# Optimization experiments

Measured on AMD Instinct MI355X. Metric: run time of the kernel, lower is better.

Reference implementation:

```python
import jax, jax.numpy as jnp
import numpy as np

N, E, D_IN, D, L = 50000, 100000, 78, 768, 5
BN_EPS = 1e-5


def setup_inputs() -> dict:
    key = jax.random.key(0)
    ks = jax.random.split(key, 8)
    s_in = 1.0 / np.sqrt(D_IN)
    s_d = 1.0 / np.sqrt(D)
    return {
        "x": jax.random.normal(ks[0], (N, D_IN), dtype=jnp.float32),
        "edge_index": jax.random.randint(ks[1], (2, E), 0, N, dtype=jnp.int32),
        "in_w": jax.random.normal(ks[2], (D_IN, D), dtype=jnp.float32) * s_in,
        "in_b": jnp.zeros((D,), jnp.float32),
        "conv_w": jax.random.normal(ks[3], (L, D, D), dtype=jnp.float32) * s_d,
        "conv_b": jnp.zeros((L, D), jnp.float32),
        "bn_g": jnp.ones((L, D), jnp.float32),
        "bn_b": jnp.zeros((L, D), jnp.float32),
        "out_w": jax.random.normal(ks[4], (D, D), dtype=jnp.float32) * s_d,
        "out_b": jnp.zeros((D,), jnp.float32),
    }


def reference(x, edge_index, in_w, in_b, conv_w, conv_b, bn_g, bn_b, out_w, out_b):
    src, dst = edge_index[0], edge_index[1]
    # GCN symmetric normalization with self-loops: deg over dst (col), +1 for self-loop
    deg = jax.ops.segment_sum(jnp.ones((E,), x.dtype), dst, num_segments=N) + 1.0
    dinv = jax.lax.rsqrt(deg)                      # deg >= 1, always finite
    edge_norm = (dinv[src] * dinv[dst])[:, None]   # [E, 1]
    self_norm = (dinv * dinv)[:, None]             # [N, 1] self-loop coefficient

    h = x @ in_w + in_b                            # input_proj -> [N, D]
    for l in range(L):
        xw = h @ conv_w[l]                         # GCNConv linear
        agg = jax.ops.segment_sum(xw[src] * edge_norm, dst, num_segments=N)
        agg = agg + xw * self_norm + conv_b[l]     # self-loop message + bias
        # BatchNorm1d (training mode: batch stats, biased variance)
        mu = jnp.mean(agg, axis=0)
        var = jnp.mean(jnp.square(agg - mu), axis=0)
        hn = (agg - mu) * jax.lax.rsqrt(var + BN_EPS) * bn_g[l] + bn_b[l]
        h = h + jax.nn.relu(hn)                    # residual (drop_ratio=0)
    return h @ out_w + out_b
```

## Files before the change

### kernel.cpp

```cpp
#include <hip/hip_runtime.h>
#include <hip/hip_bf16.h>
#include <stdint.h>

#define NN 50000
#define EE 100000
#define DD 768
#define MP 50176
#define KIN 96
#define SCB 196

typedef _Float16 half_t;
typedef __attribute__((ext_vector_type(8))) _Float16 v8h;
typedef __attribute__((ext_vector_type(4))) float v4f;

__device__ __forceinline__ void gload16(const half_t* g, half_t* l){
  __builtin_amdgcn_global_load_lds(
      (const __attribute__((address_space(1))) unsigned int*)(g),
      (__attribute__((address_space(3))) unsigned int*)(l),
      16, 0, 0);
}

template<int MODE, int KK>
__global__ __launch_bounds__(256, 3)
void gemm_t(const half_t* __restrict__ A,
            const half_t* __restrict__ Bt,
            const float* __restrict__ bias,
            float* __restrict__ o32,
            half_t* __restrict__ o16)
{
  constexpr int NKT = KK/32;
  __shared__ __align__(16) half_t lds[3*8192];

  const int nwg = gridDim.x;
  const int q = nwg >> 3, r = nwg & 7;
  const int xcd = blockIdx.x & 7, ii = blockIdx.x >> 3;
  const int L = (xcd < r ? xcd*(q+1) : r*(q+1) + (xcd-r)*q) + ii;
  const int rowb = L / 6, colb = L - rowb*6;
  const int m0 = rowb*128, n0 = colb*128;

  const int t = threadIdx.x, l = t&63, w = t>>6;
  const int wm = w>>1, wn = w&1;

  v4f acc[4][4];
  #pragma unroll
  for (int i=0;i<4;++i)
    #pragma unroll
    for (int j=0;j<4;++j){ v4f z = {0.f,0.f,0.f,0.f}; acc[i][j]=z; }

  const int srow = 16*w + (l>>2);
  const int sch  = ((l&3) ^ ((l>>3)&3))*8;
  const half_t* ApA = A  + (size_t)(m0 + srow)*KK + sch;
  const half_t* ApB = Bt + (size_t)(n0 + srow)*KK + sch;
  const int aoff = w*512;

  auto STAGE = [&](int kt2, int b){
    half_t* Ab = lds + b*8192;
    half_t* Bb = Ab + 4096;
    const int ko = kt2*32;
    gload16(ApA + ko,                  Ab + aoff);
    gload16(ApA + ko + (size_t)64*KK,  Ab + aoff + 2048);
    gload16(ApB + ko,                  Bb + aoff);
    gload16(ApB + ko + (size_t)64*KK,  Bb + aoff + 2048);
  };

  const int ra = l&15;
  const int pc = ((l>>4) ^ ((ra>>1)&3))*8;

  v8h af[2][4], bf[2][4];

  #define LOADF(s_, base_) do{                                              \
    const half_t* Ab_ = lds + (base_);                                      \
    const half_t* Bb_ = Ab_ + 4096;                                         \
    _Pragma("unroll")                                                       \
    for (int n_=0;n_<4;++n_) bf[s_][n_] = *(const v8h*)(Bb_ + (wn*64 + n_*16 + ra)*32 + pc); \
    _Pragma("unroll")                                                       \
    for (int m_=0;m_<4;++m_) af[s_][m_] = *(const v8h*)(Ab_ + (wm*64 + m_*16 + ra)*32 + pc); \
  }while(0)

  #define MFMAS(s_) do{                                                     \
    __builtin_amdgcn_s_setprio(1);                                          \
    _Pragma("unroll")                                                       \
    for (int m_=0;m_<4;++m_)                                                \
      _Pragma("unroll")                                                     \
      for (int n_=0;n_<4;++n_)                                              \
        acc[m_][n_] = __builtin_amdgcn_mfma_f32_16x16x32_f16(af[s_][m_], bf[s_][n_], acc[m_][n_], 0,0,0); \
    __builtin_amdgcn_s_setprio(0);                                          \
  }while(0)

  STAGE(0,0); STAGE(1,1); STAGE(2,2);
  asm volatile("s_waitcnt vmcnt(8)" ::: "memory");
  __builtin_amdgcn_s_barrier();
  LOADF(0, 0);
  asm volatile("s_waitcnt lgkmcnt(0)" ::: "memory");
  __builtin_amdgcn_sched_barrier(0);

  #pragma unroll
  for (int i=0;i<NKT;++i){
    const int cur = i&1, nxt = cur^1;
    if (i < NKT-1){
      if (i < NKT-2) asm volatile("s_waitcnt vmcnt(4)" ::: "memory");
      else           asm volatile("s_waitcnt vmcnt(0)" ::: "memory");
      __builtin_amdgcn_s_barrier();
      if (i+3 < NKT) STAGE(i+3, i%3);
      LOADF(nxt, ((i+1)%3)*8192);
      MFMAS(cur);
      asm volatile("s_waitcnt lgkmcnt(0)" ::: "memory");
      __builtin_amdgcn_sched_barrier(0);
    } else {
      MFMAS(cur);
    }
  }
  #undef LOADF
  #undef MFMAS

  if (MODE==2){
    float bv[4];
    #pragma unroll
    for (int n=0;n<4;++n) bv[n] = bias[n0 + wn*64 + n*16 + ra];
    #pragma unroll
    for (int m=0;m<4;++m){
      #pragma unroll
      for (int rr=0;rr<4;++rr){
        int row = m0 + wm*64 + m*16 + (l>>4)*4 + rr;
        if (row >= NN) continue;
        #pragma unroll
        for (int n=0;n<4;++n){
          int col = n0 + wn*64 + n*16 + ra;
          o32[(size_t)row*DD + col] = acc[m][n][rr] + bv[n];
        }
      }
    }
  } else {
    __syncthreads();
    #pragma unroll
    for (int m=0;m<4;++m){
      #pragma unroll
      for (int rr=0;rr<4;++rr){
        int row = wm*64 + m*16 + (l>>4)*4 + rr;
        #pragma unroll
        for (int n=0;n<4;++n){
          int col = wn*64 + n*16 + ra;
          float v = acc[m][n][rr];
          if (MODE==0) v += bias[n0+col];
          int gran = (col>>3) ^ (row&7);
          lds[row*128 + gran*8 + (col&7)] = (half_t)v;
        }
      }
    }
    __syncthreads();
    #pragma unroll
    for (int g=0; g<8; ++g){
      int row = (t>>4) + g*16;
      int gran = t&15;
      v8h hv = *(const v8h*)(lds + row*128 + ((gran ^ (row&7)))*8);
      *(v8h*)(o16 + (size_t)(m0+row)*DD + n0 + gran*8) = hv;
    }
  }
}

__global__ void k_count(const int* __restrict__ dst, int* __restrict__ cnt){
  int e = blockIdx.x*256 + threadIdx.x;
  if (e < EE) atomicAdd(&cnt[dst[e]], 1);
}
__global__ void k_dinv(const int* __restrict__ cnt, float* __restrict__ dinv){
  int i = blockIdx.x*256 + threadIdx.x;
  if (i < MP) dinv[i] = (i < NN) ? rsqrtf((float)cnt[i] + 1.0f) : 0.f;
}
__global__ void k_bsum(const int* __restrict__ cnt, int* __restrict__ bsum){
  int i = blockIdx.x*256 + threadIdx.x;
  int v = (i < NN) ? cnt[i] : 0;
  #pragma unroll
  for (int o=1;o<64;o<<=1) v += __shfl_xor(v, o);
  __shared__ int ws_[4];
  if ((threadIdx.x&63)==0) ws_[threadIdx.x>>6] = v;
  __syncthreads();
  if (threadIdx.x==0) bsum[blockIdx.x] = ws_[0]+ws_[1]+ws_[2]+ws_[3];
}
__global__ void k_btop(const int* __restrict__ bsum, int* __restrict__ boff){
  if (threadIdx.x==0){
    int run = 0;
    for (int b=0;b<SCB;++b){ boff[b] = run; run += bsum[b]; }
  }
}
__global__ void k_rowptr(const int* __restrict__ cnt, const int* __restrict__ boff,
                         int* __restrict__ rowptr, int* __restrict__ cursor){
  __shared__ int sh[256];
  int i = blockIdx.x*256 + threadIdx.x;
  int v = (i < NN) ? cnt[i] : 0;
  sh[threadIdx.x] = v; __syncthreads();
  #pragma unroll
  for (int o=1;o<256;o<<=1){
    int add = 0;
    if (threadIdx.x >= o) add = sh[threadIdx.x - o];
    __syncthreads();
    sh[threadIdx.x] += add;
    __syncthreads();
  }
  int excl = sh[threadIdx.x] - v + boff[blockIdx.x];
  if (i <= NN) rowptr[i] = excl;
  if (i < NN)  cursor[i] = excl;
}
__global__ void k_fill(const int* __restrict__ src, const int* __restrict__ dst,
                       const float* __restrict__ dinv, int* __restrict__ cursor,
                       int* __restrict__ ss, float* __restrict__ we){
  int e = blockIdx.x*256 + threadIdx.x;
  if (e < EE){
    int s = src[e], d = dst[e];
    int pos = atomicAdd(&cursor[d], 1);
    ss[pos] = s;
    we[pos] = dinv[s]*dinv[d];
  }
}
__global__ void k_x16(const float* __restrict__ x, half_t* __restrict__ x16){
  int idx = blockIdx.x*256 + threadIdx.x;
  if (idx < MP*KIN){
    int row = idx / KIN, k = idx - row*KIN;
    float v = (row < NN && k < 78) ? x[(size_t)row*78 + k] : 0.f;
    x16[idx] = (half_t)v;
  }
}
__global__ void k_tr(const float* __restrict__ src, half_t* __restrict__ dst, int K, int ldk){
  int idx = blockIdx.x*256 + threadIdx.x;
  if (idx < DD*ldk){
    int n = idx / ldk, k = idx - n*ldk;
    dst[idx] = (k < K) ? (half_t)src[(size_t)k*DD + n] : (half_t)0.f;
  }
}

__global__ __launch_bounds__(256)
void k_gather(const int* __restrict__ rowptr, const int* __restrict__ ss,
              const float* __restrict__ we, const half_t* __restrict__ xw,
              const float* __restrict__ dinv, const float* __restrict__ bias,
              half_t* __restrict__ agg16, float* __restrict__ stats){
  const int t = threadIdx.x, l = t&63, wv = t>>6;
  float b_[12];
  #pragma unroll
  for (int j=0;j<12;++j) b_[j] = bias[l + 64*j];
  float s_[12], q_[12];
  #pragma unroll
  for (int j=0;j<12;++j){ s_[j]=0.f; q_[j]=0.f; }

  for (int d = blockIdx.x*4 + wv; d < NN; d += gridDim.x*4){
    int beg = rowptr[d], end = rowptr[d+1];
    float dv = dinv[d], sn = dv*dv;
    const half_t* xr = xw + (size_t)d*DD + l;
    float a_[12];
    #pragma unroll
    for (int j=0;j<12;++j) a_[j] = fmaf(sn, (float)xr[64*j], b_[j]);
    int e = beg;
    for (; e+1 < end; e += 2){
      int sA = ss[e], sB = ss[e+1];
      float wA = we[e], wB = we[e+1];
      const half_t* xA = xw + (size_t)sA*DD + l;
      const half_t* xB = xw + (size_t)sB*DD + l;
      #pragma unroll
      for (int j=0;j<12;++j) a_[j] += wA*(float)xA[64*j] + wB*(float)xB[64*j];
    }
    if (e < end){
      int sA = ss[e]; float wA = we[e];
      const half_t* xA = xw + (size_t)sA*DD + l;
      #pragma unroll
      for (int j=0;j<12;++j) a_[j] = fmaf(wA, (float)xA[64*j], a_[j]);
    }
    half_t* ar = agg16 + (size_t)d*DD + l;
    #pragma unroll
    for (int j=0;j<12;++j) ar[64*j] = (half_t)a_[j];
    #pragma unroll
    for (int j=0;j<12;++j){ s_[j]+=a_[j]; q_[j]+=a_[j]*a_[j]; }
  }

  __shared__ float red[4][24][64];
  #pragma unroll
  for (int j=0;j<12;++j){ red[wv][j][l] = s_[j]; red[wv][12+j][l] = q_[j]; }
  __syncthreads();
  #pragma unroll
  for (int k=0;k<6;++k){
    int idx  = t + k*256;
    int slot = idx>>6, lane = idx&63;
    float v = red[0][slot][lane]+red[1][slot][lane]+red[2][slot][lane]+red[3][slot][lane];
    int off = (slot<12) ? (lane + 64*slot) : (DD + lane + 64*(slot-12));
    atomicAdd(&stats[off], v);
  }
}

__global__ void k_final(const float* __restrict__ stats, const float* __restrict__ g,
                        const float* __restrict__ b, float* __restrict__ sc, float* __restrict__ sh){
  int t = threadIdx.x;
  #pragma unroll
  for (int j=0;j<3;++j){
    int d = t + j*256;
    float mu  = stats[d]      * (1.0f/NN);
    float msq = stats[DD+d]   * (1.0f/NN);
    float var = msq - mu*mu;
    float rstd = rsqrtf(var + 1e-5f);
    float scale = rstd * g[d];
    sc[d] = scale;
    sh[d] = b[d] - mu*scale;
  }
}
__global__ void k_apply(const half_t* __restrict__ agg16, const float* __restrict__ sc,
                        const float* __restrict__ sh, half_t* __restrict__ h16){
  const int total = NN*DD/8;
  for (int i = blockIdx.x*blockDim.x + threadIdx.x; i < total; i += gridDim.x*blockDim.x){
    size_t base = (size_t)i*8;
    int col = (int)(base % DD);
    v8h a = *(const v8h*)(agg16 + base);
    v8h h = *(const v8h*)(h16 + base);
    v8h o;
    #pragma unroll
    for (int j=0;j<8;++j){
      float v = fmaxf(fmaf((float)a[j], sc[col+j], sh[col+j]), 0.f);
      o[j] = (half_t)((float)h[j] + v);
    }
    *(v8h*)(h16 + base) = o;
  }
}

extern "C" void kernel_launch(void* const* d_in, const int* in_sizes, int n_in,
                              void* d_out, int out_size, void* d_ws, size_t ws_size,
                              hipStream_t stream){
  (void)in_sizes; (void)n_in; (void)out_size; (void)ws_size;
  const float* x      = (const float*)d_in[0];
  const int*   ei     = (const int*)  d_in[1];
  const float* in_w   = (const float*)d_in[2];
  const float* in_b   = (const float*)d_in[3];
  const float* conv_w = (const float*)d_in[4];
  const float* conv_b = (const float*)d_in[5];
  const float* bn_g   = (const float*)d_in[6];
  const float* bn_b   = (const float*)d_in[7];
  const float* out_w  = (const float*)d_in[8];
  const float* out_b  = (const float*)d_in[9];
  float* out = (float*)d_out;
  const int* srcI = ei;
  const int* dstI = ei + EE;

  char* ws = (char*)d_ws; size_t off = 0;
  auto alloc = [&](size_t b)->void*{ void* p = ws + off; off += (b + 255) & ~(size_t)255; return p; };
  half_t* h16  = (half_t*)alloc((size_t)MP*DD*2);
  half_t* xw16 = (half_t*)alloc((size_t)MP*DD*2);
  half_t* agg16= (half_t*)alloc((size_t)NN*DD*2);
  half_t* x16  = (half_t*)alloc((size_t)MP*KIN*2);
  half_t* wT   = (half_t*)alloc((size_t)(DD*KIN + 6*DD*DD)*2);
  float* dinv   = (float*)alloc((size_t)MP*4);
  int*   cnt    = (int*)  alloc((size_t)MP*4);
  int*   rowptr = (int*)  alloc((size_t)(NN+1)*4);
  int*   cursor = (int*)  alloc((size_t)NN*4);
  int*   ssE    = (int*)  alloc((size_t)EE*4);
  float* weE    = (float*)alloc((size_t)EE*4);
  int*   bsum   = (int*)  alloc((size_t)SCB*4);
  int*   boff   = (int*)  alloc((size_t)SCB*4);
  float* stats  = (float*)alloc((size_t)4*DD*4);

  half_t* wTin = wT;
  half_t* wTc  = wT + DD*KIN;
  half_t* wTo  = wTc + 5*DD*DD;

  hipMemsetAsync(cnt, 0, (size_t)MP*4, stream);
  k_count<<<(EE+255)/256,256,0,stream>>>(dstI, cnt);
  k_dinv <<<(MP+255)/256,256,0,stream>>>(cnt, dinv);
  k_bsum <<<SCB,256,0,stream>>>(cnt, bsum);
  k_btop <<<1,64,0,stream>>>(bsum, boff);
  k_rowptr<<<SCB,256,0,stream>>>(cnt, boff, rowptr, cursor);
  k_fill <<<(EE+255)/256,256,0,stream>>>(srcI, dstI, dinv, cursor, ssE, weE);
  k_x16  <<<(MP*KIN+255)/256,256,0,stream>>>(x, x16);
  k_tr   <<<(DD*KIN+255)/256,256,0,stream>>>(in_w, wTin, 78, KIN);
  for (int l = 0; l < 5; ++l)
    k_tr <<<(DD*DD+255)/256,256,0,stream>>>(conv_w + (size_t)l*DD*DD, wTc + (size_t)l*DD*DD, DD, DD);
  k_tr   <<<(DD*DD+255)/256,256,0,stream>>>(out_w, wTo, DD, DD);

  const int NWG = (MP/128)*(DD/128);
  gemm_t<0,KIN><<<NWG,256,0,stream>>>(x16, wTin, in_b, nullptr, h16);

  for (int l = 0; l < 5; ++l){
    gemm_t<1,DD><<<NWG,256,0,stream>>>(h16, wTc + (size_t)l*DD*DD, nullptr, nullptr, xw16);
    hipMemsetAsync(stats, 0, (size_t)2*DD*4, stream);
    k_gather<<<2048,256,0,stream>>>(rowptr, ssE, weE, xw16, dinv, conv_b + l*DD, agg16, stats);
    k_final<<<1,256,0,stream>>>(stats, bn_g + l*DD, bn_b + l*DD, stats+2*DD, stats+3*DD);
    k_apply<<<2048,256,0,stream>>>(agg16, stats+2*DD, stats+3*DD, h16);
  }

  gemm_t<2,DD><<<NWG,256,0,stream>>>(h16, wTo, out_b, out, nullptr);
}
```

Before: 1.140 ms.

## Cut launches per layer by folding BN finalize into apply and batching transposes

Drops the per-layer stats memset and the single-block finalize kernel: k_apply now computes BN scale/shift from raw stats itself, using a fixed grid stride (1536*256 threads, a multiple of the row length) so each thread's columns stay constant. Per-layer stats buffers are zeroed once up front. The five conv weight transposes become one 2D-grid launch. The GEMM main loop is restructured to merge the vmcnt/lgkmcnt waits and drop the sched_barriers, which changes how the scheduler can interleave LDS reads with MFMAs.

```diff
diff --git a/kernel.cpp b/kernel.cpp
--- a/kernel.cpp
+++ b/kernel.cpp
@@ -90,25 +90,19 @@
   STAGE(0,0); STAGE(1,1); STAGE(2,2);
   asm volatile("s_waitcnt vmcnt(8)" ::: "memory");
   __builtin_amdgcn_s_barrier();
+  asm volatile("" ::: "memory");
   LOADF(0, 0);
-  asm volatile("s_waitcnt lgkmcnt(0)" ::: "memory");
-  __builtin_amdgcn_sched_barrier(0);
 
   #pragma unroll
   for (int i=0;i<NKT;++i){
     const int cur = i&1, nxt = cur^1;
-    if (i < NKT-1){
-      if (i < NKT-2) asm volatile("s_waitcnt vmcnt(4)" ::: "memory");
-      else           asm volatile("s_waitcnt vmcnt(0)" ::: "memory");
-      __builtin_amdgcn_s_barrier();
-      if (i+3 < NKT) STAGE(i+3, i%3);
-      LOADF(nxt, ((i+1)%3)*8192);
-      MFMAS(cur);
-      asm volatile("s_waitcnt lgkmcnt(0)" ::: "memory");
-      __builtin_amdgcn_sched_barrier(0);
-    } else {
-      MFMAS(cur);
-    }
+    if (i < NKT-2) asm volatile("s_waitcnt vmcnt(4) lgkmcnt(0)" ::: "memory");
+    else           asm volatile("s_waitcnt vmcnt(0) lgkmcnt(0)" ::: "memory");
+    __builtin_amdgcn_s_barrier();
+    asm volatile("" ::: "memory");
+    if (i+3 < NKT) STAGE(i+3, i%3);
+    if (i+1 < NKT) LOADF(nxt, ((i+1)%3)*8192);
+    MFMAS(cur);
   }
   #undef LOADF
   #undef MFMAS
@@ -226,6 +220,14 @@
     dst[idx] = (k < K) ? (half_t)src[(size_t)k*DD + n] : (half_t)0.f;
   }
 }
+__global__ void k_tr5(const float* __restrict__ src, half_t* __restrict__ dst){
+  int lidx = blockIdx.y;
+  int idx = blockIdx.x*256 + threadIdx.x;
+  if (idx < DD*DD){
+    int n = idx / DD, k = idx - n*DD;
+    dst[(size_t)lidx*DD*DD + idx] = (half_t)src[(size_t)lidx*DD*DD + (size_t)k*DD + n];
+  }
+}
 
 __global__ __launch_bounds__(256)
 void k_gather(const int* __restrict__ rowptr, const int* __restrict__ ss,
@@ -283,33 +285,32 @@
   }
 }
 
-__global__ void k_final(const float* __restrict__ stats, const float* __restrict__ g,
-                        const float* __restrict__ b, float* __restrict__ sc, float* __restrict__ sh){
-  int t = threadIdx.x;
-  #pragma unroll
-  for (int j=0;j<3;++j){
-    int d = t + j*256;
-    float mu  = stats[d]      * (1.0f/NN);
-    float msq = stats[DD+d]   * (1.0f/NN);
+__global__ __launch_bounds__(256)
+void k_apply(const half_t* __restrict__ agg16, const float* __restrict__ stats,
+             const float* __restrict__ g, const float* __restrict__ b,
+             half_t* __restrict__ h16){
+  const int tid = blockIdx.x*256 + threadIdx.x;
+  const int col = (tid*8) % DD;
+  float sc[8], sh[8];
+  #pragma unroll
+  for (int j=0;j<8;++j){
+    float mu  = stats[col+j]    * (1.0f/NN);
+    float msq = stats[DD+col+j] * (1.0f/NN);
     float var = msq - mu*mu;
     float rstd = rsqrtf(var + 1e-5f);
-    float scale = rstd * g[d];
-    sc[d] = scale;
-    sh[d] = b[d] - mu*scale;
-  }
-}
-__global__ void k_apply(const half_t* __restrict__ agg16, const float* __restrict__ sc,
-                        const float* __restrict__ sh, half_t* __restrict__ h16){
+    float scale = rstd * g[col+j];
+    sc[j] = scale;
+    sh[j] = b[col+j] - mu*scale;
+  }
   const int total = NN*DD/8;
-  for (int i = blockIdx.x*blockDim.x + threadIdx.x; i < total; i += gridDim.x*blockDim.x){
+  for (int i = tid; i < total; i += 1536*256){
     size_t base = (size_t)i*8;
-    int col = (int)(base % DD);
     v8h a = *(const v8h*)(agg16 + base);
     v8h h = *(const v8h*)(h16 + base);
     v8h o;
     #pragma unroll
     for (int j=0;j<8;++j){
-      float v = fmaxf(fmaf((float)a[j], sc[col+j], sh[col+j]), 0.f);
+      float v = fmaxf(fmaf((float)a[j], sc[j], sh[j]), 0.f);
       o[j] = (half_t)((float)h[j] + v);
     }
     *(v8h*)(h16 + base) = o;
@@ -349,13 +350,14 @@
   float* weE    = (float*)alloc((size_t)EE*4);
   int*   bsum   = (int*)  alloc((size_t)SCB*4);
   int*   boff   = (int*)  alloc((size_t)SCB*4);
-  float* stats  = (float*)alloc((size_t)4*DD*4);
+  float* stats5 = (float*)alloc((size_t)5*2*DD*4);
 
   half_t* wTin = wT;
   half_t* wTc  = wT + DD*KIN;
   half_t* wTo  = wTc + 5*DD*DD;
 
   hipMemsetAsync(cnt, 0, (size_t)MP*4, stream);
+  hipMemsetAsync(stats5, 0, (size_t)5*2*DD*4, stream);
   k_count<<<(EE+255)/256,256,0,stream>>>(dstI, cnt);
   k_dinv <<<(MP+255)/256,256,0,stream>>>(cnt, dinv);
   k_bsum <<<SCB,256,0,stream>>>(cnt, bsum);
@@ -364,19 +366,20 @@
   k_fill <<<(EE+255)/256,256,0,stream>>>(srcI, dstI, dinv, cursor, ssE, weE);
   k_x16  <<<(MP*KIN+255)/256,256,0,stream>>>(x, x16);
   k_tr   <<<(DD*KIN+255)/256,256,0,stream>>>(in_w, wTin, 78, KIN);
-  for (int l = 0; l < 5; ++l)
-    k_tr <<<(DD*DD+255)/256,256,0,stream>>>(conv_w + (size_t)l*DD*DD, wTc + (size_t)l*DD*DD, DD, DD);
+  {
+    dim3 g5((DD*DD+255)/256, 5);
+    k_tr5<<<g5,256,0,stream>>>(conv_w, wTc);
+  }
   k_tr   <<<(DD*DD+255)/256,256,0,stream>>>(out_w, wTo, DD, DD);
 
   const int NWG = (MP/128)*(DD/128);
   gemm_t<0,KIN><<<NWG,256,0,stream>>>(x16, wTin, in_b, nullptr, h16);
 
   for (int l = 0; l < 5; ++l){
+    float* statsL = stats5 + (size_t)l*2*DD;
     gemm_t<1,DD><<<NWG,256,0,stream>>>(h16, wTc + (size_t)l*DD*DD, nullptr, nullptr, xw16);
-    hipMemsetAsync(stats, 0, (size_t)2*DD*4, stream);
-    k_gather<<<2048,256,0,stream>>>(rowptr, ssE, weE, xw16, dinv, conv_b + l*DD, agg16, stats);
-    k_final<<<1,256,0,stream>>>(stats, bn_g + l*DD, bn_b + l*DD, stats+2*DD, stats+3*DD);
-    k_apply<<<2048,256,0,stream>>>(agg16, stats+2*DD, stats+3*DD, h16);
+    k_gather<<<2048,256,0,stream>>>(rowptr, ssE, weE, xw16, dinv, conv_b + l*DD, agg16, statsL);
+    k_apply<<<1536,256,0,stream>>>(agg16, statsL, bn_g + l*DD, bn_b + l*DD, h16);
   }
 
   gemm_t<2,DD><<<NWG,256,0,stream>>>(h16, wTo, out_b, out, nullptr);
```

Result: faster. 1.107 ms (-2.9%).
